# Optimization experiments

Hardware: AMD Instinct MI355X
Metric: run time of the kernel (lower is better)

## Reference

```python
import jax, jax.numpy as jnp
import numpy as np

HID = 7168; H = 128; DQ = 1536; DKV = 512; DH = 128; DR = 64; MAXS = 4096

def _rope_tables(seq_len):
    inv_freq = 1.0 / (10000.0 ** (jnp.arange(0, DR, 2, dtype=jnp.float32) / DR))
    t = jnp.arange(seq_len, dtype=jnp.float32)
    freqs = jnp.outer(t, inv_freq)              # [S, DR/2]
    emb = jnp.concatenate([freqs, freqs], -1)   # [S, DR]
    return jnp.cos(emb), jnp.sin(emb)

def _apply_rope(x, cos, sin):
    # x: [..., S, DR]; cos/sin: [S, DR]
    d = x.shape[-1]
    x1, x2 = x[..., : d // 2], x[..., d // 2 :]
    rotated = jnp.concatenate([-x2, x1], -1)
    return (x * cos + rotated * sin).astype(x.dtype)

def setup_inputs() -> dict:
    key = jax.random.key(0)
    ks = jax.random.split(key, 16)
    s = 0.02
    inp = {
        "h":    jax.random.normal(ks[0], (1, 1024, HID), jnp.float32),
        "Wdq":  jax.random.normal(ks[1], (DQ, HID), jnp.float32) * s,
        "bdq":  jnp.zeros((DQ,), jnp.float32),
        "Wdkv": jax.random.normal(ks[2], (DKV, HID), jnp.float32) * s,
        "bdkv": jnp.zeros((DKV,), jnp.float32),
        "Wuq":  jax.random.normal(ks[3], (H * DH, DQ), jnp.float32) * s,
        "buq":  jnp.zeros((H * DH,), jnp.float32),
        "Wukv": jax.random.normal(ks[4], (H * DH * 2, DKV), jnp.float32) * s,
        "bukv": jnp.zeros((H * DH * 2,), jnp.float32),
        "Wrq":  jax.random.normal(ks[5], (H * DR, DQ), jnp.float32) * s,
        "brq":  jnp.zeros((H * DR,), jnp.float32),
        "Wrk":  jax.random.normal(ks[6], (DR, HID), jnp.float32) * s,
        "brk":  jnp.zeros((DR,), jnp.float32),
        "Wo":   jax.random.normal(ks[7], (HID, H * DH), jnp.float32) * s,
        "bo":   jnp.zeros((HID,), jnp.float32),
    }
    return inp

def reference(h, Wdq, bdq, Wdkv, bdkv, Wuq, buq, Wukv, bukv, Wrq, brq, Wrk, brk, Wo, bo):
    B, S, _ = h.shape
    c_q = h @ Wdq.T + bdq              # [B,S,DQ]
    c_kv = h @ Wdkv.T + bdkv           # [B,S,DKV]
    q_c = (c_q @ Wuq.T + buq).reshape(B, S, H, DH).transpose(0, 2, 1, 3)     # [B,H,S,DH]
    kv_c = (c_kv @ Wukv.T + bukv).reshape(B, S, H, 2 * DH).transpose(0, 2, 1, 3)
    k_c, v = kv_c[..., :DH], kv_c[..., DH:]                                  # [B,H,S,DH]
    q_r = (c_q @ Wrq.T + brq).reshape(B, S, H, DR).transpose(0, 2, 1, 3)     # [B,H,S,DR]
    k_r = (h @ Wrk.T + brk).reshape(B, S, 1, DR).transpose(0, 2, 1, 3)       # [B,1,S,DR]
    cos, sin = _rope_tables(S)
    q_r = _apply_rope(q_r, cos, sin)
    k_r = _apply_rope(k_r, cos, sin)
    q = jnp.concatenate([q_c, q_r], -1)                                      # [B,H,S,DH+DR]
    k = jnp.concatenate([k_c, jnp.broadcast_to(k_r, (B, H, S, DR))], -1)
    scale = 1.0 / jnp.sqrt(jnp.float32(DH + DR))
    scores = jnp.einsum('bhqd,bhkd->bhqk', q, k) * scale
    attn = jax.nn.softmax(scores, axis=-1)
    o = jnp.einsum('bhqk,bhkd->bhqd', attn, v)        # [B,H,S,DH]
    o = o.transpose(0, 2, 1, 3).reshape(B, S, H * DH)
    return o @ Wo.T + bo
```

## Files before the change

kernel.cpp:

```cpp
#include <hip/hip_runtime.h>
#include <hip/hip_bf16.h>

#define S_LEN 1024
#define HID 7168
#define NH 128
#define DQ 1536
#define DKV 512
#define DH 128
#define DR 64

typedef __attribute__((ext_vector_type(8))) short bf16x8;
typedef __attribute__((ext_vector_type(4))) float f32x4;
typedef __attribute__((ext_vector_type(4))) float fl4;
typedef __attribute__((ext_vector_type(4))) unsigned short us4;
typedef __attribute__((ext_vector_type(8))) unsigned short us8;
typedef __attribute__((ext_vector_type(4))) unsigned int u32x4;

static __device__ __forceinline__ unsigned short f2bf(float f) {
  union { float f; unsigned int u; } v; v.f = f;
  unsigned int u = v.u;
  return (unsigned short)((u + 0x7fffu + ((u >> 16) & 1u)) >> 16);
}
static __device__ __forceinline__ float bf2f(unsigned short u) {
  union { unsigned int u; float f; } v; v.u = ((unsigned int)u) << 16;
  return v.f;
}
static __device__ __forceinline__ unsigned int cvtpk2(float lo, float hi) {
  unsigned int r;
  asm("v_cvt_pk_bf16_f32 %0, %1, %2" : "=v"(r) : "v"(lo), "v"(hi));
  return r;
}

__global__ __launch_bounds__(256) void cvt_bf16_kernel(
    const float* __restrict__ in, unsigned short* __restrict__ out, int n8) {
  int i = blockIdx.x * 256 + threadIdx.x;
  int stride = gridDim.x * 256;
  for (; i < n8; i += stride) {
    fl4 a = ((const fl4*)in)[2 * i];
    fl4 b = ((const fl4*)in)[2 * i + 1];
    us8 u = { f2bf(a[0]), f2bf(a[1]), f2bf(a[2]), f2bf(a[3]),
              f2bf(b[0]), f2bf(b[1]), f2bf(b[2]), f2bf(b[3]) };
    ((us8*)out)[i] = u;
  }
}

template <int OUTMODE, int WFP32>
__global__ __launch_bounds__(256) void gemm_k(
    const unsigned short* __restrict__ A, int lda,
    const unsigned short* __restrict__ Wb16,
    const float* __restrict__ Wfa, const float* __restrict__ Wfb, int nsplit,
    int ldw,
    const float* __restrict__ bias,
    void* __restrict__ Cv, int ldc, size_t zstride,
    int Ncl, int ksl, float alpha)
{
  const int n0 = blockIdx.x * 128;
  if (n0 >= Ncl) return;

  __shared__ unsigned short As[128 * 64];
  __shared__ unsigned short Ws[128 * 64];
  const int t = threadIdx.x;
  const int l = t & 63, w = t >> 6;
  const int r15 = l & 15, g = l >> 4;
  const int wm = (w >> 1) * 64, wn = (w & 1) * 64;
  const int m0 = blockIdx.y * 128;
  const int kbase = blockIdx.z * ksl;
  const int srow = l >> 3;
  const int scol = (l & 7) * 8;

  f32x4 acc[4][4];
#pragma unroll
  for (int i = 0; i < 4; ++i)
#pragma unroll
    for (int j = 0; j < 4; ++j) acc[i][j] = (f32x4){0.f, 0.f, 0.f, 0.f};

  const unsigned short* Ab = A + (size_t)m0 * lda;
  const unsigned short* Wb = nullptr;
  const float* Wf = nullptr;
  if constexpr (WFP32) {
    Wf = (n0 < nsplit) ? Wfa + (size_t)n0 * ldw : Wfb + (size_t)(n0 - nsplit) * ldw;
  } else {
    Wb = Wb16 + (size_t)n0 * ldw;
  }

  fl4 wx[4], wy[4];
  auto issueW = [&](int k0) {
#pragma unroll
    for (int i = 0; i < 4; ++i) {
      int c = t + 256 * i;
      const float* src = Wf + (size_t)(c >> 3) * ldw + k0 + (c & 7) * 8;
      wx[i] = *(const fl4*)src;
      wy[i] = *(const fl4*)(src + 4);
    }
  };

  if constexpr (WFP32) issueW(kbase);
  const int kend = kbase + ksl;

  for (int k0 = kbase; k0 < kend; k0 += 64) {
    __syncthreads();
#pragma unroll
    for (int i = 0; i < 4; ++i) {
      int chunk = w * 4 + i;
      int row = chunk * 8 + srow;
      __builtin_amdgcn_global_load_lds(
          (const __attribute__((address_space(1))) void*)(Ab + (size_t)row * lda + k0 + scol),
          (__attribute__((address_space(3))) void*)(As + chunk * 512), 16, 0, 0);
      if constexpr (!WFP32) {
        __builtin_amdgcn_global_load_lds(
            (const __attribute__((address_space(1))) void*)(Wb + (size_t)row * ldw + k0 + scol),
            (__attribute__((address_space(3))) void*)(Ws + chunk * 512), 16, 0, 0);
      }
    }
    if constexpr (WFP32) {
#pragma unroll
      for (int i = 0; i < 4; ++i) {
        int c = t + 256 * i;
        u32x4 p = { cvtpk2(wx[i][0], wx[i][1]), cvtpk2(wx[i][2], wx[i][3]),
                    cvtpk2(wy[i][0], wy[i][1]), cvtpk2(wy[i][2], wy[i][3]) };
        ((u32x4*)Ws)[c] = p;
      }
    }
    __syncthreads();
    if constexpr (WFP32) {
      if (k0 + 64 < kend) issueW(k0 + 64);
    }
#pragma unroll
    for (int kk = 0; kk < 2; ++kk) {
      bf16x8 a[4], b[4];
#pragma unroll
      for (int mt = 0; mt < 4; ++mt)
        a[mt] = *reinterpret_cast<const bf16x8*>(&As[(wm + mt * 16 + r15) * 64 + kk * 32 + 8 * g]);
#pragma unroll
      for (int nt = 0; nt < 4; ++nt)
        b[nt] = *reinterpret_cast<const bf16x8*>(&Ws[(wn + nt * 16 + r15) * 64 + kk * 32 + 8 * g]);
#pragma unroll
      for (int mt = 0; mt < 4; ++mt)
#pragma unroll
        for (int nt = 0; nt < 4; ++nt)
          acc[mt][nt] = __builtin_amdgcn_mfma_f32_16x16x32_bf16(a[mt], b[nt], acc[mt][nt], 0, 0, 0);
    }
  }

  if constexpr (OUTMODE == 1) {
    float bv[4];
#pragma unroll
    for (int nt = 0; nt < 4; ++nt) {
      int col = n0 + wn + nt * 16 + r15;
      bv[nt] = (col < Ncl) ? bias[col] : 0.f;
    }
#pragma unroll
    for (int mt = 0; mt < 4; ++mt)
#pragma unroll
      for (int nt = 0; nt < 4; ++nt) {
        int col = n0 + wn + nt * 16 + r15;
        if (col < Ncl) {
#pragma unroll
          for (int r = 0; r < 4; ++r) {
            int row = m0 + wm + mt * 16 + g * 4 + r;
            ((unsigned short*)Cv)[(size_t)row * ldc + col] =
                f2bf((acc[mt][nt][r] + bv[nt]) * alpha);
          }
        }
      }
  } else {
    float* Cp = (float*)Cv + blockIdx.z * zstride;
#pragma unroll
    for (int mt = 0; mt < 4; ++mt)
#pragma unroll
      for (int nt = 0; nt < 4; ++nt) {
        int col = n0 + wn + nt * 16 + r15;
        if (col < Ncl) {
#pragma unroll
          for (int r = 0; r < 4; ++r) {
            int row = m0 + wm + mt * 16 + g * 4 + r;
            Cp[(size_t)row * ldc + col] = acc[mt][nt][r];
          }
        }
      }
  }
}

__global__ __launch_bounds__(256) void reduce_f32_kernel(
    const float* __restrict__ pbuf, const float* __restrict__ bias,
    float* __restrict__ out, int ldo, int rowlen4, int nz, size_t zstride, int total4)
{
  int idx = blockIdx.x * 256 + threadIdx.x;
  if (idx >= total4) return;
  int r = idx / rowlen4, c4 = idx % rowlen4;
  fl4 acc = *(const fl4*)(bias + c4 * 4);
  for (int z = 0; z < nz; ++z)
    acc += *(const fl4*)(pbuf + z * zstride + (size_t)idx * 4);
  *(fl4*)(out + (size_t)r * ldo + c4 * 4) = acc;
}

__global__ __launch_bounds__(256) void reduce_bf16_kernel(
    const float* __restrict__ pbuf, const float* __restrict__ bias,
    unsigned short* __restrict__ out, int ldo, int rowlen4, int nz, size_t zstride, int total4)
{
  int idx = blockIdx.x * 256 + threadIdx.x;
  if (idx >= total4) return;
  int r = idx / rowlen4, c4 = idx % rowlen4;
  fl4 acc = *(const fl4*)(bias + c4 * 4);
  for (int z = 0; z < nz; ++z)
    acc += *(const fl4*)(pbuf + z * zstride + (size_t)idx * 4);
  us4 u = { f2bf(acc[0]), f2bf(acc[1]), f2bf(acc[2]), f2bf(acc[3]) };
  *(us4*)(out + (size_t)r * ldo + c4 * 4) = u;
}

__global__ __launch_bounds__(256) void rope_table_kernel(float* __restrict__ ctab,
                                                         float* __restrict__ stab) {
  int idx = blockIdx.x * 256 + threadIdx.x;
  if (idx >= S_LEN * 32) return;
  int j = idx & 31, s = idx >> 5;
  float invf = expf(-0.28782313662425574f * (float)j);
  float ang = (float)s * invf;
  ctab[idx] = cosf(ang);
  stab[idx] = sinf(ang);
}

__global__ void rope_bf16_kernel(unsigned short* __restrict__ x, int nh, int lda, int total,
                                 const float* __restrict__ ctab,
                                 const float* __restrict__ stab) {
  int idx = blockIdx.x * 256 + threadIdx.x;
  if (idx >= total) return;
  int j = idx & 31;
  int rest = idx >> 5;
  int hh = rest % nh;
  int s = rest / nh;
  float c = ctab[s * 32 + j], sn = stab[s * 32 + j];
  size_t base = (size_t)s * lda + hh * 64;
  float x1 = bf2f(x[base + j]), x2 = bf2f(x[base + j + 32]);
  x[base + j]      = f2bf(x1 * c - x2 * sn);
  x[base + j + 32] = f2bf(x2 * c + x1 * sn);
}

__global__ __launch_bounds__(256) void vtrans_kernel(
    const unsigned short* __restrict__ kvb, unsigned short* __restrict__ vt) {
  __shared__ unsigned short tl[64][72];
  const int s0 = blockIdx.x * 64;
  const int c0 = blockIdx.y * 64;
  const int t = threadIdx.x;
  const int rr = t >> 3, cc = (t & 7) * 8;
  const int hbase = (c0 >> 7) * 256 + 128 + (c0 & 127);
#pragma unroll
  for (int i = 0; i < 2; ++i) {
    int r = rr + i * 32;
    *reinterpret_cast<bf16x8*>(&tl[r][cc]) =
        *reinterpret_cast<const bf16x8*>(kvb + (size_t)(s0 + r) * 32768 + hbase + cc);
  }
  __syncthreads();
#pragma unroll
  for (int i = 0; i < 2; ++i) {
    int vc = rr + i * 32;
    unsigned short tmp[8];
#pragma unroll
    for (int j = 0; j < 8; ++j) tmp[j] = tl[cc + j][vc];
    *reinterpret_cast<bf16x8*>(&vt[(size_t)(c0 + vc) * 1024 + s0 + cc]) =
        *reinterpret_cast<bf16x8*>(tmp);
  }
}

__global__ __launch_bounds__(256) void mla_attn_kernel(
    const unsigned short* __restrict__ qcat,
    const unsigned short* __restrict__ kvb,
    const unsigned short* __restrict__ kr,
    const unsigned short* __restrict__ vt,
    unsigned short* __restrict__ obuf)
{
  __shared__ unsigned short Klds[64][200];
  __shared__ unsigned short Vlds[128][72];
  __shared__ unsigned short Plds[4][16][72];

  const int t = threadIdx.x;
  const int l = t & 63, w = t >> 6;
  const int r15 = l & 15, g = l >> 4;
  const int bid = blockIdx.x;
  const int orig = (bid & 7) * 256 + (bid >> 3);
  const int h = orig >> 4;
  const int q0 = (orig & 15) * 64;

  bf16x8 qf[6];
  const unsigned short* qrow = qcat + (size_t)(q0 + w * 16 + r15) * 24576;
#pragma unroll
  for (int kk = 0; kk < 4; ++kk)
    qf[kk] = *reinterpret_cast<const bf16x8*>(qrow + h * 128 + kk * 32 + 8 * g);
#pragma unroll
  for (int kk = 4; kk < 6; ++kk)
    qf[kk] = *reinterpret_cast<const bf16x8*>(qrow + 16384 + h * 64 + (kk - 4) * 32 + 8 * g);

  bf16x8 kreg[6], vreg[4];
  auto loadKV = [&](int kk0) {
#pragma unroll
    for (int i = 0; i < 6; ++i) {
      int c = t + 256 * i, row = c / 24, cb = c % 24;
      const unsigned short* src = (cb < 16)
          ? kvb + (size_t)(kk0 + row) * 32768 + h * 256 + cb * 8
          : kr + (size_t)(kk0 + row) * 2112 + (cb - 16) * 8;
      kreg[i] = *reinterpret_cast<const bf16x8*>(src);
    }
#pragma unroll
    for (int i = 0; i < 4; ++i) {
      int c = t + 256 * i, d = c >> 3, kb = c & 7;
      vreg[i] = *reinterpret_cast<const bf16x8*>(vt + ((size_t)h * 128 + d) * 1024 + kk0 + kb * 8);
    }
  };

  float m_r[4], l_r[4];
  f32x4 oacc[8];
#pragma unroll
  for (int r = 0; r < 4; ++r) { m_r[r] = -1e30f; l_r[r] = 0.f; }
#pragma unroll
  for (int d = 0; d < 8; ++d) oacc[d] = (f32x4){0.f, 0.f, 0.f, 0.f};

  loadKV(0);

  for (int kt = 0; kt < 16; ++kt) {
    __syncthreads();
#pragma unroll
    for (int i = 0; i < 6; ++i) {
      int c = t + 256 * i, row = c / 24, cb = c % 24;
      *reinterpret_cast<bf16x8*>(&Klds[row][cb * 8]) = kreg[i];
    }
#pragma unroll
    for (int i = 0; i < 4; ++i) {
      int c = t + 256 * i, d = c >> 3, kb = c & 7;
      *reinterpret_cast<bf16x8*>(&Vlds[d][kb * 8]) = vreg[i];
    }
    __syncthreads();
    if (kt < 15) loadKV((kt + 1) * 64);

    f32x4 sacc[4];
#pragma unroll
    for (int nt = 0; nt < 4; ++nt) sacc[nt] = (f32x4){0.f, 0.f, 0.f, 0.f};
    __builtin_amdgcn_s_setprio(1);
#pragma unroll
    for (int nt = 0; nt < 4; ++nt)
#pragma unroll
      for (int kk = 0; kk < 6; ++kk) {
        bf16x8 b = *reinterpret_cast<const bf16x8*>(&Klds[nt * 16 + r15][kk * 32 + 8 * g]);
        sacc[nt] = __builtin_amdgcn_mfma_f32_16x16x32_bf16(qf[kk], b, sacc[nt], 0, 0, 0);
      }
    __builtin_amdgcn_s_setprio(0);

    float sc[4], rsum[4];
#pragma unroll
    for (int r = 0; r < 4; ++r) {
      float mx = fmaxf(fmaxf(sacc[0][r], sacc[1][r]), fmaxf(sacc[2][r], sacc[3][r]));
      mx = fmaxf(mx, __shfl_xor(mx, 1));
      mx = fmaxf(mx, __shfl_xor(mx, 2));
      mx = fmaxf(mx, __shfl_xor(mx, 4));
      mx = fmaxf(mx, __shfl_xor(mx, 8));
      float mn = fmaxf(m_r[r], mx);
      sc[r] = __expf(m_r[r] - mn);
      m_r[r] = mn;
      rsum[r] = 0.f;
    }
#pragma unroll
    for (int nt = 0; nt < 4; ++nt)
#pragma unroll
      for (int r = 0; r < 4; ++r) {
        float p = __expf(sacc[nt][r] - m_r[r]);
        rsum[r] += p;
        Plds[w][g * 4 + r][nt * 16 + r15] = f2bf(p);
      }
#pragma unroll
    for (int r = 0; r < 4; ++r) {
      float s = rsum[r];
      s += __shfl_xor(s, 1);
      s += __shfl_xor(s, 2);
      s += __shfl_xor(s, 4);
      s += __shfl_xor(s, 8);
      l_r[r] = l_r[r] * sc[r] + s;
    }
#pragma unroll
    for (int d = 0; d < 8; ++d)
#pragma unroll
      for (int r = 0; r < 4; ++r) oacc[d][r] *= sc[r];

    bf16x8 pa0 = *reinterpret_cast<const bf16x8*>(&Plds[w][r15][8 * g]);
    bf16x8 pa1 = *reinterpret_cast<const bf16x8*>(&Plds[w][r15][32 + 8 * g]);
    __builtin_amdgcn_s_setprio(1);
#pragma unroll
    for (int dt = 0; dt < 8; ++dt) {
      bf16x8 v0 = *reinterpret_cast<const bf16x8*>(&Vlds[dt * 16 + r15][8 * g]);
      bf16x8 v1 = *reinterpret_cast<const bf16x8*>(&Vlds[dt * 16 + r15][32 + 8 * g]);
      oacc[dt] = __builtin_amdgcn_mfma_f32_16x16x32_bf16(pa0, v0, oacc[dt], 0, 0, 0);
      oacc[dt] = __builtin_amdgcn_mfma_f32_16x16x32_bf16(pa1, v1, oacc[dt], 0, 0, 0);
    }
    __builtin_amdgcn_s_setprio(0);
  }

#pragma unroll
  for (int dt = 0; dt < 8; ++dt)
#pragma unroll
    for (int r = 0; r < 4; ++r) {
      int row = q0 + w * 16 + g * 4 + r;
      int col = h * DH + dt * 16 + r15;
      obuf[(size_t)row * 16384 + col] = f2bf(oacc[dt][r] / l_r[r]);
    }
}

extern "C" void kernel_launch(void* const* d_in, const int* in_sizes, int n_in,
                              void* d_out, int out_size, void* d_ws, size_t ws_size,
                              hipStream_t stream) {
  const float* h    = (const float*)d_in[0];
  const float* Wdq  = (const float*)d_in[1];
  const float* bdq  = (const float*)d_in[2];
  const float* Wdkv = (const float*)d_in[3];
  const float* bdkv = (const float*)d_in[4];
  const float* Wuq  = (const float*)d_in[5];
  const float* buq  = (const float*)d_in[6];
  const float* Wukv = (const float*)d_in[7];
  const float* bukv = (const float*)d_in[8];
  const float* Wrq  = (const float*)d_in[9];
  const float* brq  = (const float*)d_in[10];
  const float* Wrk  = (const float*)d_in[11];
  const float* brk  = (const float*)d_in[12];
  const float* Wo   = (const float*)d_in[13];
  const float* bo   = (const float*)d_in[14];
  float* out = (float*)d_out;

  char* ws = (char*)d_ws;
  size_t off = 0;
  auto alloc = [&](size_t bytes) {
    char* p = ws + off;
    off += (bytes + 255) & ~(size_t)255;
    return p;
  };
  unsigned short* hb    = (unsigned short*)alloc((size_t)1024 * 7168 * 2);
  unsigned short* W1cat = (unsigned short*)alloc((size_t)2176 * 7168 * 2);
  float*          b1cat = (float*)alloc(2176 * 4);
  unsigned short* ccat  = (unsigned short*)alloc((size_t)1024 * 2112 * 2);
  float*          b2cat = (float*)alloc(24576 * 4);
  unsigned short* qcat  = (unsigned short*)alloc((size_t)1024 * 24576 * 2);
  unsigned short* kvbb  = (unsigned short*)alloc((size_t)1024 * 32768 * 2);
  unsigned short* vt    = (unsigned short*)alloc((size_t)16384 * 1024 * 2);
  unsigned short* obuf  = (unsigned short*)alloc((size_t)1024 * 16384 * 2);
  float*          ctab  = (float*)alloc((size_t)S_LEN * 32 * 4);
  float*          stab  = (float*)alloc((size_t)S_LEN * 32 * 4);
  float* pbufG1 = (float*)qcat;
  float* pbufG4 = (float*)qcat;

  auto cvt = [&](const float* in, unsigned short* outp, size_t n) {
    int n8 = (int)(n / 8);
    int blocks = (n8 + 255) / 256;
    if (blocks > 2048) blocks = 2048;
    cvt_bf16_kernel<<<blocks, 256, 0, stream>>>(in, outp, n8);
  };

  cvt(h,    hb,    (size_t)1024 * 7168);
  cvt(Wdq,  W1cat, (size_t)1536 * 7168);
  cvt(Wdkv, W1cat + (size_t)1536 * 7168, (size_t)512 * 7168);
  cvt(Wrk,  W1cat + (size_t)2048 * 7168, (size_t)64 * 7168);
  hipMemsetAsync(W1cat + (size_t)2112 * 7168, 0, (size_t)64 * 7168 * 2, stream);
  hipMemcpyAsync(b1cat,        bdq,  1536 * 4, hipMemcpyDeviceToDevice, stream);
  hipMemcpyAsync(b1cat + 1536, bdkv, 512 * 4,  hipMemcpyDeviceToDevice, stream);
  hipMemcpyAsync(b1cat + 2048, brk,  64 * 4,   hipMemcpyDeviceToDevice, stream);
  hipMemsetAsync(b1cat + 2112, 0, 64 * 4, stream);
  hipMemcpyAsync(b2cat,         buq, 16384 * 4, hipMemcpyDeviceToDevice, stream);
  hipMemcpyAsync(b2cat + 16384, brq, 8192 * 4,  hipMemcpyDeviceToDevice, stream);
  rope_table_kernel<<<(S_LEN * 32 + 255) / 256, 256, 0, stream>>>(ctab, stab);

  const float scale = 0.07216878364870323f;
  const int BIGN = 1 << 30;
  dim3 blk(256);

  gemm_k<2, 0><<<dim3(24, 8, 4), blk, 0, stream>>>(
      hb, 7168, W1cat, nullptr, nullptr, BIGN, 7168, nullptr,
      pbufG1, 2112, (size_t)1024 * 2112, 2112, 1792, 1.0f);
  reduce_bf16_kernel<<<2112, blk, 0, stream>>>(pbufG1, b1cat, ccat, 2112, 528, 4,
                                               (size_t)1024 * 2112, 1024 * 2112 / 4);
  rope_bf16_kernel<<<(1024 * 32 + 255) / 256, blk, 0, stream>>>(ccat + 2048, 1, 2112, 1024 * 32, ctab, stab);

  gemm_k<1, 1><<<dim3(192, 8, 1), blk, 0, stream>>>(
      ccat, 2112, nullptr, Wuq, Wrq, 16384, 1536, b2cat,
      qcat, 24576, 0, 24576, 1536, scale);
  rope_bf16_kernel<<<(1024 * 128 * 32 + 255) / 256, blk, 0, stream>>>(qcat + 16384, 128, 24576, 1024 * 128 * 32, ctab, stab);

  gemm_k<1, 1><<<dim3(256, 8, 1), blk, 0, stream>>>(
      ccat + 1536, 2112, nullptr, Wukv, Wukv, BIGN, 512, bukv,
      kvbb, 32768, 0, 32768, 512, 1.0f);
  vtrans_kernel<<<dim3(16, 256), blk, 0, stream>>>(kvbb, vt);
  mla_attn_kernel<<<dim3(2048), blk, 0, stream>>>(qcat, kvbb, ccat + 2048, vt, obuf);

  gemm_k<2, 1><<<dim3(56, 8, 4), blk, 0, stream>>>(
      obuf, 16384, nullptr, Wo, Wo, BIGN, 16384, nullptr,
      pbufG4, 7168, (size_t)1024 * 7168, 7168, 4096, 1.0f);
  reduce_f32_kernel<<<7168, blk, 0, stream>>>(pbufG4, bo, out,
                                              7168, 1792, 4, (size_t)1024 * 7168, 1024 * 7168 / 4);
}
```

Before: 1.135 ms.

## Replace split-K output projection with dedicated 128x64 tile GEMM fusing bias

Replaces the split-K (4-way) output projection GEMM and its separate reduction kernel with a single dedicated kernel using 128x64 tiles, 896 blocks, and full K=16384 per block. Bias is added in the epilogue and results are written directly to the output. This removes the partial-sum buffer writes and reads and one launch. In exchange each block runs a long serial K loop with smaller tiles, a single-stage LDS pipeline, and weight fp32-to-bf16 conversion in registers, so weight traffic per output tile is higher.

```diff
diff --git a/kernel.cpp b/kernel.cpp
--- a/kernel.cpp
+++ b/kernel.cpp
@@ -181,17 +181,92 @@
   }
 }
 
-__global__ __launch_bounds__(256) void reduce_f32_kernel(
-    const float* __restrict__ pbuf, const float* __restrict__ bias,
-    float* __restrict__ out, int ldo, int rowlen4, int nz, size_t zstride, int total4)
+__global__ __launch_bounds__(256, 4) void gemm_g4(
+    const unsigned short* __restrict__ A,
+    const float* __restrict__ W,
+    const float* __restrict__ bias,
+    float* __restrict__ C)
 {
-  int idx = blockIdx.x * 256 + threadIdx.x;
-  if (idx >= total4) return;
-  int r = idx / rowlen4, c4 = idx % rowlen4;
-  fl4 acc = *(const fl4*)(bias + c4 * 4);
-  for (int z = 0; z < nz; ++z)
-    acc += *(const fl4*)(pbuf + z * zstride + (size_t)idx * 4);
-  *(fl4*)(out + (size_t)r * ldo + c4 * 4) = acc;
+  __shared__ unsigned short As[128 * 64];
+  __shared__ unsigned short Ws[64 * 64];
+  const int t = threadIdx.x;
+  const int l = t & 63, w = t >> 6;
+  const int r15 = l & 15, g = l >> 4;
+  const int wm = (w >> 1) * 64;
+  const int wn = (w & 1) * 32;
+  const int n0 = blockIdx.x * 64;
+  const int m0 = blockIdx.y * 128;
+  const int srow = l >> 3;
+  const int scol = (l & 7) * 8;
+
+  f32x4 acc[4][2];
+#pragma unroll
+  for (int i = 0; i < 4; ++i)
+#pragma unroll
+    for (int j = 0; j < 2; ++j) acc[i][j] = (f32x4){0.f, 0.f, 0.f, 0.f};
+
+  const unsigned short* Ab = A + (size_t)m0 * 16384;
+  const float* Wb = W + (size_t)n0 * 16384;
+
+  fl4 wp[4];
+  const float* wsrc0 = Wb + (size_t)(t >> 2) * 16384 + (t & 3) * 16;
+  auto issueW = [&](int k0) {
+    const float* src = wsrc0 + k0;
+#pragma unroll
+    for (int q = 0; q < 4; ++q) wp[q] = *(const fl4*)(src + q * 4);
+  };
+  issueW(0);
+
+  for (int k0 = 0; k0 < 16384; k0 += 64) {
+    __syncthreads();
+#pragma unroll
+    for (int i = 0; i < 4; ++i) {
+      int chunk = w * 4 + i;
+      int row = chunk * 8 + srow;
+      __builtin_amdgcn_global_load_lds(
+          (const __attribute__((address_space(1))) void*)(Ab + (size_t)row * 16384 + k0 + scol),
+          (__attribute__((address_space(3))) void*)(As + chunk * 512), 16, 0, 0);
+    }
+    {
+      u32x4 p0 = { cvtpk2(wp[0][0], wp[0][1]), cvtpk2(wp[0][2], wp[0][3]),
+                   cvtpk2(wp[1][0], wp[1][1]), cvtpk2(wp[1][2], wp[1][3]) };
+      u32x4 p1 = { cvtpk2(wp[2][0], wp[2][1]), cvtpk2(wp[2][2], wp[2][3]),
+                   cvtpk2(wp[3][0], wp[3][1]), cvtpk2(wp[3][2], wp[3][3]) };
+      unsigned short* dst = Ws + (t >> 2) * 64 + (t & 3) * 16;
+      *(u32x4*)dst = p0;
+      *(u32x4*)(dst + 8) = p1;
+    }
+    __syncthreads();
+    if (k0 + 64 < 16384) issueW(k0 + 64);
+#pragma unroll
+    for (int kk = 0; kk < 2; ++kk) {
+      bf16x8 a[4], b[2];
+#pragma unroll
+      for (int mt = 0; mt < 4; ++mt)
+        a[mt] = *reinterpret_cast<const bf16x8*>(&As[(wm + mt * 16 + r15) * 64 + kk * 32 + 8 * g]);
+#pragma unroll
+      for (int nt = 0; nt < 2; ++nt)
+        b[nt] = *reinterpret_cast<const bf16x8*>(&Ws[(wn + nt * 16 + r15) * 64 + kk * 32 + 8 * g]);
+#pragma unroll
+      for (int mt = 0; mt < 4; ++mt)
+#pragma unroll
+        for (int nt = 0; nt < 2; ++nt)
+          acc[mt][nt] = __builtin_amdgcn_mfma_f32_16x16x32_bf16(a[mt], b[nt], acc[mt][nt], 0, 0, 0);
+    }
+  }
+
+  float bv[2] = { bias[n0 + wn + r15], bias[n0 + wn + 16 + r15] };
+#pragma unroll
+  for (int mt = 0; mt < 4; ++mt)
+#pragma unroll
+    for (int nt = 0; nt < 2; ++nt) {
+      int col = n0 + wn + nt * 16 + r15;
+#pragma unroll
+      for (int r = 0; r < 4; ++r) {
+        int row = m0 + wm + mt * 16 + g * 4 + r;
+        C[(size_t)row * 7168 + col] = acc[mt][nt][r] + bv[nt];
+      }
+    }
 }
 
 __global__ __launch_bounds__(256) void reduce_bf16_kernel(
@@ -440,7 +515,6 @@
   float*          ctab  = (float*)alloc((size_t)S_LEN * 32 * 4);
   float*          stab  = (float*)alloc((size_t)S_LEN * 32 * 4);
   float* pbufG1 = (float*)qcat;
-  float* pbufG4 = (float*)qcat;
 
   auto cvt = [&](const float* in, unsigned short* outp, size_t n) {
     int n8 = (int)(n / 8);
@@ -484,9 +558,5 @@
   vtrans_kernel<<<dim3(16, 256), blk, 0, stream>>>(kvbb, vt);
   mla_attn_kernel<<<dim3(2048), blk, 0, stream>>>(qcat, kvbb, ccat + 2048, vt, obuf);
 
-  gemm_k<2, 1><<<dim3(56, 8, 4), blk, 0, stream>>>(
-      obuf, 16384, nullptr, Wo, Wo, BIGN, 16384, nullptr,
-      pbufG4, 7168, (size_t)1024 * 7168, 7168, 4096, 1.0f);
-  reduce_f32_kernel<<<7168, blk, 0, stream>>>(pbufG4, bo, out,
-                                              7168, 1792, 4, (size_t)1024 * 7168, 1024 * 7168 / 4);
-}
+  gemm_g4<<<dim3(112, 8), blk, 0, stream>>>(obuf, Wo, bo, out);
+}
```

After: 1.222 ms. 1.08x slower.
